# Kernel tuning notes

Measured on AMD Instinct MI355X. Metric: run time of the kernel, lower is better.

## Reference

```python
import jax, jax.numpy as jnp
import numpy as np

B, N, C, H = 8, 1024, 768, 12
D = C // H  # 64
LAMBDA_INIT = 0.8 - 0.6 * np.exp(-0.3 * (1 - 1))  # layer_idx=1 -> 0.2
EPS = 1e-5


def setup_inputs() -> dict:
    key = jax.random.key(0)
    ks = jax.random.split(key, 8)
    s = 0.02
    return {
        "x": jax.random.normal(ks[0], (B, N, C), dtype=jnp.float32),
        "Wq": jax.random.normal(ks[1], (C, 2 * C), dtype=jnp.float32) * s,
        "Wk": jax.random.normal(ks[2], (C, 2 * C), dtype=jnp.float32) * s,
        "Wv": jax.random.normal(ks[3], (C, 2 * C), dtype=jnp.float32) * s,
        "lam": jnp.float32(1.0),
        "gamma": jnp.ones((2 * D,), dtype=jnp.float32),
        "beta": jnp.zeros((2 * D,), dtype=jnp.float32),
        "Wp": jax.random.normal(ks[4], (2 * C, C), dtype=jnp.float32) * s,
        "bp": jnp.zeros((C,), dtype=jnp.float32),
    }


def reference(x, Wq, Wk, Wv, lam, gamma, beta, Wp, bp):
    scale = D ** -0.5
    # project to double-width qkv, split heads: (B, H, N, 2D)
    q = (x @ Wq).reshape(B, N, H, 2 * D).transpose(0, 2, 1, 3)
    k = (x @ Wk).reshape(B, N, H, 2 * D).transpose(0, 2, 1, 3)
    v = (x @ Wv).reshape(B, N, H, 2 * D).transpose(0, 2, 1, 3)
    q1, q2 = jnp.split(q, 2, axis=-1)
    k1, k2 = jnp.split(k, 2, axis=-1)
    a1 = jax.nn.softmax(jnp.einsum("bhnd,bhmd->bhnm", q1, k1) * scale, axis=-1)
    a2 = jax.nn.softmax(jnp.einsum("bhnd,bhmd->bhnm", q2, k2) * scale, axis=-1)
    # lambda-weighted differential attention, then apply to double-width V
    out = jnp.einsum("bhnm,bhmd->bhnd", a1 - lam * a2, v)  # (B, H, N, 2D)
    # LayerNorm over the 2D channel dim
    mu = out.mean(axis=-1, keepdims=True)
    var = out.var(axis=-1, keepdims=True)
    out = (out - mu) * jax.lax.rsqrt(var + EPS) * gamma + beta
    out = out * (1.0 - LAMBDA_INIT)
    out = out.transpose(0, 2, 1, 3).reshape(B, N, 2 * C)
    return out @ Wp + bp
```

## Files before the change

kernel.cpp:

```cpp
#include <hip/hip_runtime.h>

#define B_ 8
#define N_ 1024
#define C_ 768
#define H_ 12
#define BH_ 96
#define D2_ 128
#define C2_ 1536

static constexpr float SCALE_LOG2 = 0.125f * 1.4426950408889634f;
static constexpr float OUT_SCALE  = 0.8f;
static constexpr float EPS_       = 1e-5f;

using bf16x8 = __attribute__((ext_vector_type(8))) short;
using f32x4  = __attribute__((ext_vector_type(4))) float;
typedef unsigned short ushort_t;
typedef unsigned int   uint_t;

#define GLOAD16(g, l) __builtin_amdgcn_global_load_lds( \
    (const __attribute__((address_space(1))) void*)(g), \
    (__attribute__((address_space(3))) void*)(l), 16, 0, 0)

__device__ __forceinline__ ushort_t f2bf(float f) {
    uint_t u = __float_as_uint(f);
    u = (u + 0x7FFFu + ((u >> 16) & 1u)) >> 16;
    return (ushort_t)u;
}
__device__ __forceinline__ uint_t packbf(float a, float b) {
    return (uint_t)f2bf(a) | ((uint_t)f2bf(b) << 16);
}

__global__ __launch_bounds__(256) void cvt_bf16_kernel(const float* __restrict__ in,
                                                       ushort_t* __restrict__ out, int n4) {
    for (int i = blockIdx.x * 256 + threadIdx.x; i < n4; i += gridDim.x * 256) {
        float4 v = reinterpret_cast<const float4*>(in)[i];
        ushort4 o;
        o.x = f2bf(v.x); o.y = f2bf(v.y); o.z = f2bf(v.z); o.w = f2bf(v.w);
        reinterpret_cast<ushort4*>(out)[i] = o;
    }
}

__global__ __launch_bounds__(256) void transpose_cvt_kernel(const float* __restrict__ W,
                                                            ushort_t* __restrict__ Wt,
                                                            int K, int Nn) {
    __shared__ float t[32][33];
    const int n0 = blockIdx.x * 32, k0 = blockIdx.y * 32;
    const int tx = threadIdx.x & 31, ty = threadIdx.x >> 5;
    #pragma unroll
    for (int r = ty; r < 32; r += 8)
        t[r][tx] = W[(size_t)(k0 + r) * Nn + n0 + tx];
    __syncthreads();
    #pragma unroll
    for (int r = ty; r < 32; r += 8)
        Wt[(size_t)(n0 + r) * K + k0 + tx] = f2bf(t[tx][r]);
}

__global__ __launch_bounds__(256) void transpose_v_kernel(const ushort_t* __restrict__ V,
                                                          ushort_t* __restrict__ Vt) {
    __shared__ ushort_t t[64][65];
    const int bh = blockIdx.z;
    const int d0 = blockIdx.x * 64, n0 = blockIdx.y * 64;
    const int tx = threadIdx.x & 63, ty = threadIdx.x >> 6;
    const ushort_t* src = V + (size_t)bh * N_ * D2_;
    ushort_t* dst = Vt + (size_t)bh * N_ * D2_;
    #pragma unroll
    for (int r = ty; r < 64; r += 4)
        t[r][tx] = src[(size_t)(n0 + r) * D2_ + d0 + tx];
    __syncthreads();
    #pragma unroll
    for (int r = ty; r < 64; r += 4)
        dst[(size_t)(d0 + r) * N_ + n0 + tx] = t[tx][r];
}

template <int REMAP>
__global__ __launch_bounds__(256)
void gemm_bf16_kernel(const ushort_t* __restrict__ A, const ushort_t* __restrict__ Bt,
                      const float* __restrict__ bias, void* __restrict__ dst,
                      int M, int Nn, int K)
{
    __shared__ __align__(16) char As[8192];
    __shared__ __align__(16) char Bs[8192];
    const int tid = threadIdx.x;
    const int wv = tid >> 6, lane = tid & 63;
    const int l15 = lane & 15, lg = lane >> 4;
    const int m0 = blockIdx.y * 128, n0 = blockIdx.x * 128;
    const int wm = (wv >> 1) * 64, wn = (wv & 1) * 64;

    f32x4 acc[4][4] = {};
    const size_t ldb = (size_t)K * 2;

    for (int k0 = 0; k0 < K; k0 += 32) {
        __syncthreads();
        #pragma unroll
        for (int q = 0; q < 2; ++q) {
            const int o = wv * 2048 + q * 1024 + lane * 16;
            const int sw = (o & 63) ^ ((((o >> 7) & 3)) << 4);
            const char* sa = (const char*)A + (size_t)(m0 + (o >> 6)) * ldb + k0 * 2 + sw;
            const char* sb = (const char*)Bt + (size_t)(n0 + (o >> 6)) * ldb + k0 * 2 + sw;
            GLOAD16(sa, As + wv * 2048 + q * 1024);
            GLOAD16(sb, Bs + wv * 2048 + q * 1024);
        }
        __syncthreads();
        bf16x8 af[4], bfr[4];
        #pragma unroll
        for (int i = 0; i < 4; ++i) {
            const int ra = wm + i * 16 + l15;
            af[i] = *(const bf16x8*)(As + ra * 64 + ((lg ^ ((ra >> 1) & 3)) << 4));
            const int rb = wn + i * 16 + l15;
            bfr[i] = *(const bf16x8*)(Bs + rb * 64 + ((lg ^ ((rb >> 1) & 3)) << 4));
        }
        #pragma unroll
        for (int i = 0; i < 4; ++i)
            #pragma unroll
            for (int j = 0; j < 4; ++j)
                acc[i][j] = __builtin_amdgcn_mfma_f32_16x16x32_bf16(af[i], bfr[j], acc[i][j], 0, 0, 0);
    }

    if (REMAP) {
        ushort_t* D = (ushort_t*)dst;
        #pragma unroll
        for (int i = 0; i < 4; ++i)
            #pragma unroll
            for (int r = 0; r < 4; ++r) {
                const int m = m0 + wm + i * 16 + lg * 4 + r;
                const int b = m >> 10, ns = m & 1023;
                #pragma unroll
                for (int j = 0; j < 4; ++j) {
                    const int n = n0 + wn + j * 16 + l15;
                    const int h = n >> 7, d = n & 127;
                    D[(((size_t)(b * H_ + h)) * N_ + ns) * D2_ + d] = f2bf(acc[i][j][r]);
                }
            }
    } else {
        float* D = (float*)dst;
        #pragma unroll
        for (int i = 0; i < 4; ++i)
            #pragma unroll
            for (int r = 0; r < 4; ++r) {
                const int m = m0 + wm + i * 16 + lg * 4 + r;
                #pragma unroll
                for (int j = 0; j < 4; ++j) {
                    const int n = n0 + wn + j * 16 + l15;
                    D[(size_t)m * Nn + n] = acc[i][j][r] + bias[n];
                }
            }
    }
}

__global__ __launch_bounds__(256)
void attn_kernel(const ushort_t* __restrict__ qb, const ushort_t* __restrict__ kb,
                 const ushort_t* __restrict__ vt, const float* __restrict__ lamp,
                 const float* __restrict__ gamma, const float* __restrict__ beta,
                 ushort_t* __restrict__ Y)
{
    __shared__ __align__(16) char Ks[2][32 * 272];
    __shared__ __align__(16) char Vs[2][128 * 80];
    __shared__ __align__(16) ushort_t Ps[4][2][16 * 40];

    const int tid = threadIdx.x;
    const int wv = tid >> 6, lane = tid & 63;
    const int l15 = lane & 15, lg = lane >> 4;
    const int swz = (blockIdx.x & 7) * 192 + (blockIdx.x >> 3);
    const int bh = swz >> 4;
    const int qt = swz & 15;

    const char* kbase = (const char*)kb + (size_t)bh * (N_ * D2_ * 2);
    const char* vbase = (const char*)vt + (size_t)bh * (N_ * D2_ * 2);

    const int krow = tid >> 4, kcol = tid & 15;
    const int kg0 = tid * 16, kg1 = kg0 + 4096;
    const int kw0 = krow * 272 + kcol * 16;
    const int kw1 = (krow + 16) * 272 + kcol * 16;
    const int vdr = tid >> 2, vpart = tid & 3;
    const size_t vg0 = (size_t)vdr * (N_ * 2) + vpart * 16;
    const size_t vg1 = (size_t)(vdr + 64) * (N_ * 2) + vpart * 16;
    const int vw0 = vdr * 80 + vpart * 16;
    const int vw1 = (vdr + 64) * 80 + vpart * 16;

    const int qrow = qt * 64 + wv * 16 + l15;
    const ushort_t* qptr = qb + (size_t)bh * N_ * D2_ + (size_t)qrow * D2_;
    bf16x8 Qf[4];
    #pragma unroll
    for (int c = 0; c < 4; ++c)
        Qf[c] = *(const bf16x8*)(qptr + c * 32 + lg * 8);

    f32x4 O1[8] = {}, O2[8] = {};
    float l1p = 0.f, l2p = 0.f;

    {
        uint4 a = *(const uint4*)(kbase + kg0);
        uint4 b = *(const uint4*)(kbase + kg1);
        uint4 c = *(const uint4*)(vbase + vg0);
        uint4 d = *(const uint4*)(vbase + vg1);
        *(uint4*)(Ks[0] + kw0) = a; *(uint4*)(Ks[0] + kw1) = b;
        *(uint4*)(Vs[0] + vw0) = c; *(uint4*)(Vs[0] + vw1) = d;
    }
    __syncthreads();
    int cur = 0;

    for (int t = 0; t < 32; ++t) {
        uint4 nk0, nk1, nv0, nv1;
        if (t < 31) {
            nk0 = *(const uint4*)(kbase + (t + 1) * 8192 + kg0);
            nk1 = *(const uint4*)(kbase + (t + 1) * 8192 + kg1);
            nv0 = *(const uint4*)(vbase + vg0 + (t + 1) * 64);
            nv1 = *(const uint4*)(vbase + vg1 + (t + 1) * 64);
        }

        const char* Kc = Ks[cur];
        const char* Vc = Vs[cur];

        f32x4 s1[2], s2[2];
        #pragma unroll
        for (int u = 0; u < 2; ++u) {
            const int row = u * 16 + l15;
            const char* kp = Kc + row * 272;
            bf16x8 k0 = *(const bf16x8*)(kp + (0  + lg) * 16);
            bf16x8 k1 = *(const bf16x8*)(kp + (4  + lg) * 16);
            bf16x8 k2 = *(const bf16x8*)(kp + (8  + lg) * 16);
            bf16x8 k3 = *(const bf16x8*)(kp + (12 + lg) * 16);
            f32x4 z = {0.f, 0.f, 0.f, 0.f};
            s1[u] = __builtin_amdgcn_mfma_f32_16x16x32_bf16(k0, Qf[0], z, 0, 0, 0);
            s1[u] = __builtin_amdgcn_mfma_f32_16x16x32_bf16(k1, Qf[1], s1[u], 0, 0, 0);
            s2[u] = __builtin_amdgcn_mfma_f32_16x16x32_bf16(k2, Qf[2], z, 0, 0, 0);
            s2[u] = __builtin_amdgcn_mfma_f32_16x16x32_bf16(k3, Qf[3], s2[u], 0, 0, 0);
        }

        float lp1 = 0.f, lp2 = 0.f;
        #pragma unroll
        for (int u = 0; u < 2; ++u) {
            const uint_t base = (uint_t)(l15 * 40 + u * 16 + lg * 4) >> 1;
            float a0 = exp2f(s1[u][0] * SCALE_LOG2), a1 = exp2f(s1[u][1] * SCALE_LOG2);
            float a2 = exp2f(s1[u][2] * SCALE_LOG2), a3 = exp2f(s1[u][3] * SCALE_LOG2);
            lp1 += (a0 + a1) + (a2 + a3);
            ((uint_t*)Ps[wv][0])[base]     = packbf(a0, a1);
            ((uint_t*)Ps[wv][0])[base + 1] = packbf(a2, a3);
            float b0 = exp2f(s2[u][0] * SCALE_LOG2), b1 = exp2f(s2[u][1] * SCALE_LOG2);
            float b2 = exp2f(s2[u][2] * SCALE_LOG2), b3 = exp2f(s2[u][3] * SCALE_LOG2);
            lp2 += (b0 + b1) + (b2 + b3);
            ((uint_t*)Ps[wv][1])[base]     = packbf(b0, b1);
            ((uint_t*)Ps[wv][1])[base + 1] = packbf(b2, b3);
        }
        l1p += lp1; l2p += lp2;

        bf16x8 pa1 = *(const bf16x8*)&Ps[wv][0][l15 * 40 + lg * 8];
        bf16x8 pa2 = *(const bf16x8*)&Ps[wv][1][l15 * 40 + lg * 8];

        #pragma unroll
        for (int c = 0; c < 8; ++c) {
            const int dr = c * 16 + l15;
            bf16x8 vf = *(const bf16x8*)(Vc + dr * 80 + lg * 16);
            O1[c] = __builtin_amdgcn_mfma_f32_16x16x32_bf16(pa1, vf, O1[c], 0, 0, 0);
            O2[c] = __builtin_amdgcn_mfma_f32_16x16x32_bf16(pa2, vf, O2[c], 0, 0, 0);
        }

        if (t < 31) {
            char* Kn = Ks[cur ^ 1];
            char* Vn = Vs[cur ^ 1];
            *(uint4*)(Kn + kw0) = nk0; *(uint4*)(Kn + kw1) = nk1;
            *(uint4*)(Vn + vw0) = nv0; *(uint4*)(Vn + vw1) = nv1;
        }
        __syncthreads();
        cur ^= 1;
    }

    float l1 = l1p + __shfl_xor(l1p, 16); l1 += __shfl_xor(l1, 32);
    float l2 = l2p + __shfl_xor(l2p, 16); l2 += __shfl_xor(l2, 32);
    const float lam = lamp[0];
    float i1[4], i2[4];
    #pragma unroll
    for (int r = 0; r < 4; ++r) {
        i1[r] = 1.f / __shfl(l1, lg * 4 + r);
        i2[r] = lam / __shfl(l2, lg * 4 + r);
    }
    float su[4] = {0.f, 0.f, 0.f, 0.f}, sq[4] = {0.f, 0.f, 0.f, 0.f};
    float ov[8][4];
    #pragma unroll
    for (int c = 0; c < 8; ++c)
        #pragma unroll
        for (int r = 0; r < 4; ++r) {
            const float v = O1[c][r] * i1[r] - O2[c][r] * i2[r];
            ov[c][r] = v; su[r] += v; sq[r] += v * v;
        }
    #pragma unroll
    for (int r = 0; r < 4; ++r) {
        #pragma unroll
        for (int msk = 1; msk <= 8; msk <<= 1) {
            su[r] += __shfl_xor(su[r], msk);
            sq[r] += __shfl_xor(sq[r], msk);
        }
    }
    float gv[8], bv[8];
    #pragma unroll
    for (int c = 0; c < 8; ++c) { gv[c] = gamma[c * 16 + l15]; bv[c] = beta[c * 16 + l15]; }

    const int b = bh / H_, h = bh - (bh / H_) * H_;
    #pragma unroll
    for (int r = 0; r < 4; ++r) {
        const float mu = su[r] * (1.f / 128.f);
        const float var = sq[r] * (1.f / 128.f) - mu * mu;
        const float rstd = rsqrtf(var + EPS_);
        const int n = qt * 64 + wv * 16 + lg * 4 + r;
        ushort_t* yrow = Y + ((size_t)(b * N_ + n)) * C2_ + h * D2_;
        #pragma unroll
        for (int c = 0; c < 8; ++c) {
            const int d = c * 16 + l15;
            const float val = ((ov[c][r] - mu) * rstd * gv[c] + bv[c]) * OUT_SCALE;
            yrow[d] = f2bf(val);
        }
    }
}

extern "C" void kernel_launch(void* const* d_in, const int* in_sizes, int n_in,
                              void* d_out, int out_size, void* d_ws, size_t ws_size,
                              hipStream_t stream) {
    const float* x     = (const float*)d_in[0];
    const float* Wq    = (const float*)d_in[1];
    const float* Wk    = (const float*)d_in[2];
    const float* Wv    = (const float*)d_in[3];
    const float* lam   = (const float*)d_in[4];
    const float* gamma = (const float*)d_in[5];
    const float* beta  = (const float*)d_in[6];
    const float* Wp    = (const float*)d_in[7];
    const float* bp    = (const float*)d_in[8];
    float* out = (float*)d_out;

    char* w = (char*)d_ws;
    ushort_t* xb  = (ushort_t*)w;                 w += (size_t)B_ * N_ * C_ * 2;
    ushort_t* wqt = (ushort_t*)w;                 w += (size_t)C2_ * C_ * 2;
    ushort_t* wkt = (ushort_t*)w;                 w += (size_t)C2_ * C_ * 2;
    ushort_t* wvt = (ushort_t*)w;                 w += (size_t)C2_ * C_ * 2;
    ushort_t* wpt = (ushort_t*)w;                 w += (size_t)C_ * C2_ * 2;
    ushort_t* qbuf = (ushort_t*)w;                w += (size_t)BH_ * N_ * D2_ * 2;
    ushort_t* kbuf = (ushort_t*)w;                w += (size_t)BH_ * N_ * D2_ * 2;
    ushort_t* vbuf = (ushort_t*)w;                w += (size_t)BH_ * N_ * D2_ * 2;
    ushort_t* vtb  = (ushort_t*)w;                w += (size_t)BH_ * N_ * D2_ * 2;
    ushort_t* Yb   = (ushort_t*)w;                w += (size_t)B_ * N_ * C2_ * 2;

    const int M = B_ * N_;

    cvt_bf16_kernel<<<2048, 256, 0, stream>>>(x, xb, (B_ * N_ * C_) / 4);
    transpose_cvt_kernel<<<dim3(C2_ / 32, C_ / 32), 256, 0, stream>>>(Wq, wqt, C_, C2_);
    transpose_cvt_kernel<<<dim3(C2_ / 32, C_ / 32), 256, 0, stream>>>(Wk, wkt, C_, C2_);
    transpose_cvt_kernel<<<dim3(C2_ / 32, C_ / 32), 256, 0, stream>>>(Wv, wvt, C_, C2_);
    transpose_cvt_kernel<<<dim3(C_ / 32, C2_ / 32), 256, 0, stream>>>(Wp, wpt, C2_, C_);

    {
        dim3 grid(C2_ / 128, M / 128);
        gemm_bf16_kernel<1><<<grid, 256, 0, stream>>>(xb, wqt, nullptr, qbuf, M, C2_, C_);
        gemm_bf16_kernel<1><<<grid, 256, 0, stream>>>(xb, wkt, nullptr, kbuf, M, C2_, C_);
        gemm_bf16_kernel<1><<<grid, 256, 0, stream>>>(xb, wvt, nullptr, vbuf, M, C2_, C_);
    }
    transpose_v_kernel<<<dim3(D2_ / 64, N_ / 64, BH_), 256, 0, stream>>>(vbuf, vtb);

    attn_kernel<<<dim3(BH_ * (N_ / 64)), 256, 0, stream>>>(qbuf, kbuf, vtb, lam, gamma, beta, Yb);

    {
        dim3 grid(C_ / 128, M / 128);
        gemm_bf16_kernel<0><<<grid, 256, 0, stream>>>(Yb, wpt, bp, out, M, C_, C2_);
    }
}
```

Baseline: 314.7 us.

## Fuse QKV GEMMs, fold softmax scale into Q, swizzle attention LDS

The three Q/K/V projection GEMMs become one launch over a 3x wider N dimension. This relies on the transposed weights and the q/k/v output buffers being laid out back to back, and the epilogue picks the output buffer from the column block. The softmax scale (times log2 e) is applied to Q in the GEMM epilogue, so the attention kernel drops a multiply per exp2. The padded K/V shared-memory tiles are replaced by XOR-swizzled unpadded tiles, and the hand-written bf16 pack is replaced by the hardware v_cvt_pk_bf16_f32 instruction. Rounding Q to bf16 after scaling slightly changes numerics, and the fused GEMM depends on the buffer adjacency staying as it is.

```diff
diff --git a/kernel.cpp b/kernel.cpp
--- a/kernel.cpp
+++ b/kernel.cpp
@@ -26,8 +26,10 @@
     u = (u + 0x7FFFu + ((u >> 16) & 1u)) >> 16;
     return (ushort_t)u;
 }
-__device__ __forceinline__ uint_t packbf(float a, float b) {
-    return (uint_t)f2bf(a) | ((uint_t)f2bf(b) << 16);
+__device__ __forceinline__ uint_t cvtpk(float a, float b) {
+    uint_t r;
+    asm("v_cvt_pk_bf16_f32 %0, %1, %2" : "=v"(r) : "v"(a), "v"(b));
+    return r;
 }
 
 __global__ __launch_bounds__(256) void cvt_bf16_kernel(const float* __restrict__ in,
@@ -76,7 +78,7 @@
 __global__ __launch_bounds__(256)
 void gemm_bf16_kernel(const ushort_t* __restrict__ A, const ushort_t* __restrict__ Bt,
                       const float* __restrict__ bias, void* __restrict__ dst,
-                      int M, int Nn, int K)
+                      int M, int Nn, int K, float qscale)
 {
     __shared__ __align__(16) char As[8192];
     __shared__ __align__(16) char Bs[8192];
@@ -117,7 +119,10 @@
     }
 
     if (REMAP) {
-        ushort_t* D = (ushort_t*)dst;
+        const int p = n0 / C2_;
+        const float os = (p == 0) ? qscale : 1.0f;
+        ushort_t* D = (ushort_t*)dst + (size_t)p * ((size_t)BH_ * N_ * D2_);
+        const int nb = n0 - p * C2_;
         #pragma unroll
         for (int i = 0; i < 4; ++i)
             #pragma unroll
@@ -126,9 +131,9 @@
                 const int b = m >> 10, ns = m & 1023;
                 #pragma unroll
                 for (int j = 0; j < 4; ++j) {
-                    const int n = n0 + wn + j * 16 + l15;
+                    const int n = nb + wn + j * 16 + l15;
                     const int h = n >> 7, d = n & 127;
-                    D[(((size_t)(b * H_ + h)) * N_ + ns) * D2_ + d] = f2bf(acc[i][j][r]);
+                    D[(((size_t)(b * H_ + h)) * N_ + ns) * D2_ + d] = f2bf(acc[i][j][r] * os);
                 }
             }
     } else {
@@ -153,8 +158,8 @@
                  const float* __restrict__ gamma, const float* __restrict__ beta,
                  ushort_t* __restrict__ Y)
 {
-    __shared__ __align__(16) char Ks[2][32 * 272];
-    __shared__ __align__(16) char Vs[2][128 * 80];
+    __shared__ __align__(16) char Ks[2][8192];
+    __shared__ __align__(16) char Vs[2][8192];
     __shared__ __align__(16) ushort_t Ps[4][2][16 * 40];
 
     const int tid = threadIdx.x;
@@ -169,13 +174,15 @@
 
     const int krow = tid >> 4, kcol = tid & 15;
     const int kg0 = tid * 16, kg1 = kg0 + 4096;
-    const int kw0 = krow * 272 + kcol * 16;
-    const int kw1 = (krow + 16) * 272 + kcol * 16;
+    const int ksw = (kcol ^ (krow & 7)) << 4;
+    const int kw0 = krow * 256 + ksw;
+    const int kw1 = (krow + 16) * 256 + ksw;
     const int vdr = tid >> 2, vpart = tid & 3;
     const size_t vg0 = (size_t)vdr * (N_ * 2) + vpart * 16;
     const size_t vg1 = (size_t)(vdr + 64) * (N_ * 2) + vpart * 16;
-    const int vw0 = vdr * 80 + vpart * 16;
-    const int vw1 = (vdr + 64) * 80 + vpart * 16;
+    const int vsw = (vpart ^ ((vdr >> 1) & 3)) << 4;
+    const int vw0 = vdr * 64 + vsw;
+    const int vw1 = (vdr + 64) * 64 + vsw;
 
     const int qrow = qt * 64 + wv * 16 + l15;
     const ushort_t* qptr = qb + (size_t)bh * N_ * D2_ + (size_t)qrow * D2_;
@@ -214,11 +221,11 @@
         #pragma unroll
         for (int u = 0; u < 2; ++u) {
             const int row = u * 16 + l15;
-            const char* kp = Kc + row * 272;
-            bf16x8 k0 = *(const bf16x8*)(kp + (0  + lg) * 16);
-            bf16x8 k1 = *(const bf16x8*)(kp + (4  + lg) * 16);
-            bf16x8 k2 = *(const bf16x8*)(kp + (8  + lg) * 16);
-            bf16x8 k3 = *(const bf16x8*)(kp + (12 + lg) * 16);
+            const char* kp = Kc + row * 256;
+            bf16x8 k0 = *(const bf16x8*)(kp + (((0  + lg) ^ (row & 7)) << 4));
+            bf16x8 k1 = *(const bf16x8*)(kp + (((4  + lg) ^ (row & 7)) << 4));
+            bf16x8 k2 = *(const bf16x8*)(kp + (((8  + lg) ^ (row & 7)) << 4));
+            bf16x8 k3 = *(const bf16x8*)(kp + (((12 + lg) ^ (row & 7)) << 4));
             f32x4 z = {0.f, 0.f, 0.f, 0.f};
             s1[u] = __builtin_amdgcn_mfma_f32_16x16x32_bf16(k0, Qf[0], z, 0, 0, 0);
             s1[u] = __builtin_amdgcn_mfma_f32_16x16x32_bf16(k1, Qf[1], s1[u], 0, 0, 0);
@@ -230,16 +237,16 @@
         #pragma unroll
         for (int u = 0; u < 2; ++u) {
             const uint_t base = (uint_t)(l15 * 40 + u * 16 + lg * 4) >> 1;
-            float a0 = exp2f(s1[u][0] * SCALE_LOG2), a1 = exp2f(s1[u][1] * SCALE_LOG2);
-            float a2 = exp2f(s1[u][2] * SCALE_LOG2), a3 = exp2f(s1[u][3] * SCALE_LOG2);
+            float a0 = exp2f(s1[u][0]), a1 = exp2f(s1[u][1]);
+            float a2 = exp2f(s1[u][2]), a3 = exp2f(s1[u][3]);
             lp1 += (a0 + a1) + (a2 + a3);
-            ((uint_t*)Ps[wv][0])[base]     = packbf(a0, a1);
-            ((uint_t*)Ps[wv][0])[base + 1] = packbf(a2, a3);
-            float b0 = exp2f(s2[u][0] * SCALE_LOG2), b1 = exp2f(s2[u][1] * SCALE_LOG2);
-            float b2 = exp2f(s2[u][2] * SCALE_LOG2), b3 = exp2f(s2[u][3] * SCALE_LOG2);
+            ((uint_t*)Ps[wv][0])[base]     = cvtpk(a0, a1);
+            ((uint_t*)Ps[wv][0])[base + 1] = cvtpk(a2, a3);
+            float b0 = exp2f(s2[u][0]), b1 = exp2f(s2[u][1]);
+            float b2 = exp2f(s2[u][2]), b3 = exp2f(s2[u][3]);
             lp2 += (b0 + b1) + (b2 + b3);
-            ((uint_t*)Ps[wv][1])[base]     = packbf(b0, b1);
-            ((uint_t*)Ps[wv][1])[base + 1] = packbf(b2, b3);
+            ((uint_t*)Ps[wv][1])[base]     = cvtpk(b0, b1);
+            ((uint_t*)Ps[wv][1])[base + 1] = cvtpk(b2, b3);
         }
         l1p += lp1; l2p += lp2;
 
@@ -249,7 +256,7 @@
         #pragma unroll
         for (int c = 0; c < 8; ++c) {
             const int dr = c * 16 + l15;
-            bf16x8 vf = *(const bf16x8*)(Vc + dr * 80 + lg * 16);
+            bf16x8 vf = *(const bf16x8*)(Vc + dr * 64 + ((lg ^ ((dr >> 1) & 3)) << 4));
             O1[c] = __builtin_amdgcn_mfma_f32_16x16x32_bf16(pa1, vf, O1[c], 0, 0, 0);
             O2[c] = __builtin_amdgcn_mfma_f32_16x16x32_bf16(pa2, vf, O2[c], 0, 0, 0);
         }
@@ -346,17 +353,17 @@
     transpose_cvt_kernel<<<dim3(C_ / 32, C2_ / 32), 256, 0, stream>>>(Wp, wpt, C2_, C_);
 
     {
-        dim3 grid(C2_ / 128, M / 128);
-        gemm_bf16_kernel<1><<<grid, 256, 0, stream>>>(xb, wqt, nullptr, qbuf, M, C2_, C_);
-        gemm_bf16_kernel<1><<<grid, 256, 0, stream>>>(xb, wkt, nullptr, kbuf, M, C2_, C_);
-        gemm_bf16_kernel<1><<<grid, 256, 0, stream>>>(xb, wvt, nullptr, vbuf, M, C2_, C_);
-    }
+        dim3 grid((3 * C2_) / 128, M / 128);
+        gemm_bf16_kernel<1><<<grid, 256, 0, stream>>>(xb, wqt, nullptr, qbuf,
+                                                      M, 3 * C2_, C_, SCALE_LOG2);
+    }
+    (void)kbuf;
     transpose_v_kernel<<<dim3(D2_ / 64, N_ / 64, BH_), 256, 0, stream>>>(vbuf, vtb);
 
     attn_kernel<<<dim3(BH_ * (N_ / 64)), 256, 0, stream>>>(qbuf, kbuf, vtb, lam, gamma, beta, Yb);
 
     {
         dim3 grid(C_ / 128, M / 128);
-        gemm_bf16_kernel<0><<<grid, 256, 0, stream>>>(Yb, wpt, bp, out, M, C_, C2_);
-    }
-}
+        gemm_bf16_kernel<0><<<grid, 256, 0, stream>>>(Yb, wpt, bp, out, M, C_, C2_, 1.0f);
+    }
+}
```

Measured after the change: 286.6 us. 1.1x faster.
